# Optimization experiments

Measured on AMD Instinct MI355X. Metric: run time of the kernel, lower is better.

The kernel has to match this reference:

```python
import jax, jax.numpy as jnp
import numpy as np

B, S, D, Q = 8, 4096, 1024, 16  # batch, seq, embed_dim, n_qubits==ffn_dim


def setup_inputs() -> dict:
    key = jax.random.key(0)
    k = jax.random.split(key, 5)
    x = jax.random.normal(k[0], (B, S, D), dtype=jnp.float32)
    W1 = jax.random.normal(k[1], (D, Q), dtype=jnp.float32) * 0.02
    b1 = jnp.zeros((Q,), dtype=jnp.float32)
    theta = jax.random.normal(k[2], (Q,), dtype=jnp.float32)
    W2 = jax.random.normal(k[3], (Q, D), dtype=jnp.float32) * 0.02
    b2 = jnp.zeros((D,), dtype=jnp.float32)
    return {"x": x, "W1": W1, "b1": b1, "theta": theta, "W2": W2, "b2": b2}


def reference(x, W1, b1, theta, W2, b2):
    # linear1 + ReLU (dropout is identity in eval mode)
    h = jax.nn.relu(jnp.einsum("bsd,dq->bsq", x, W1) + b1)  # [B,S,Q] angles
    # QLayer: RY(h_i) then RY(theta_i) on wire i from |0>; rotations on the
    # same wire compose additively and <Z> after RY(a)|0> is cos(a), so
    # MeasureAll(PauliZ) == cos(h + theta) per wire (exact, product state).
    z = jnp.cos(h + theta)  # [B,S,Q]
    # linear2
    return jnp.einsum("bsq,qd->bsd", z, W2) + b2
```

## Files before the change

### kernel.cpp

```cpp
#include <hip/hip_runtime.h>
#include <math.h>
#include <stdint.h>

#define ROWS_TOTAL 32768
#define DDIM 1024
#define QDIM 16

typedef __attribute__((ext_vector_type(8))) short bf16x8;
typedef __attribute__((ext_vector_type(4))) float f32x4;

union ABfrag { uint32_t u[4]; bf16x8 v; };

__device__ __forceinline__ uint32_t packhi(uint32_t a, uint32_t b) {
  return __builtin_amdgcn_perm(b, a, 0x07060302u);
}

#define ZTPB 512
#define ZWPB 8
#define ZNBLOCKS (ROWS_TOTAL / 16)

__global__ __launch_bounds__(ZTPB, 4)
void z_kernel(const float* __restrict__ x, const float* __restrict__ W1,
              const float* __restrict__ b1, const float* __restrict__ theta,
              float* __restrict__ z, int zstride) {
  const int t    = threadIdx.x;
  const int lane = t & 63;
  const int wid  = t >> 6;
  const int g    = lane >> 4;
  const int q5   = lane & 15;

  __shared__ __align__(16) float xs[16][DDIM];
  __shared__ __align__(16) float red[ZWPB][64][4];

  const int row0 = blockIdx.x * 16;
  const int kb   = wid * 128;

  const float bq = b1[q5];
  const float tq = theta[q5];

  float wf[4][8];
#pragma unroll
  for (int s = 0; s < 4; ++s) {
    const float* wp = W1 + (size_t)(kb + 32 * s + 4 * g) * QDIM + q5;
#pragma unroll
    for (int j = 0; j < 4; ++j) wf[s][j] = wp[(size_t)j * QDIM];
#pragma unroll
    for (int j = 0; j < 4; ++j) wf[s][4 + j] = wp[(size_t)(16 + j) * QDIM];
  }

  f32x4 st[8];
  {
    const int rs = 2 * wid;
#pragma unroll
    for (int rr = 0; rr < 2; ++rr) {
      const float* xp = x + (size_t)(row0 + rs + rr) * DDIM;
#pragma unroll
      for (int p = 0; p < 4; ++p)
        st[rr * 4 + p] = __builtin_nontemporal_load(
            reinterpret_cast<const f32x4*>(xp + 4 * (64 * p + lane)));
    }
#pragma unroll
    for (int rr = 0; rr < 2; ++rr) {
      const int r = rs + rr;
#pragma unroll
      for (int p = 0; p < 4; ++p) {
        const int u = 64 * p + lane;
        *reinterpret_cast<f32x4*>(&xs[r][4 * (u ^ (r & 7))]) = st[rr * 4 + p];
      }
    }
  }

  ABfrag bhi[4], blo[4];
#pragma unroll
  for (int s = 0; s < 4; ++s) {
    uint32_t u[8], lo[8];
#pragma unroll
    for (int j = 0; j < 8; ++j) {
      u[j]  = __float_as_uint(wf[s][j]);
      lo[j] = __float_as_uint(wf[s][j] - __uint_as_float(u[j] & 0xFFFF0000u));
    }
    bhi[s].u[0] = packhi(u[0], u[1]);   bhi[s].u[1] = packhi(u[2], u[3]);
    bhi[s].u[2] = packhi(u[4], u[5]);   bhi[s].u[3] = packhi(u[6], u[7]);
    blo[s].u[0] = packhi(lo[0], lo[1]); blo[s].u[1] = packhi(lo[2], lo[3]);
    blo[s].u[2] = packhi(lo[4], lo[5]); blo[s].u[3] = packhi(lo[6], lo[7]);
  }

  __syncthreads();

  const int rr = lane & 15;
  const int ub = 32 * wid;
  float4 a0[4], a1[4];
#pragma unroll
  for (int s = 0; s < 4; ++s) {
    a0[s] = *reinterpret_cast<const float4*>(
        &xs[rr][4 * ((ub + 8 * s + g) ^ (rr & 7))]);
    a1[s] = *reinterpret_cast<const float4*>(
        &xs[rr][4 * ((ub + 8 * s + 4 + g) ^ (rr & 7))]);
  }

  f32x4 acc = {0.f, 0.f, 0.f, 0.f};
#pragma unroll
  for (int s = 0; s < 4; ++s) {
    const float fv[8] = {a0[s].x, a0[s].y, a0[s].z, a0[s].w,
                         a1[s].x, a1[s].y, a1[s].z, a1[s].w};
    uint32_t u[8], lo[8];
#pragma unroll
    for (int j = 0; j < 8; ++j) {
      u[j]  = __float_as_uint(fv[j]);
      lo[j] = __float_as_uint(fv[j] - __uint_as_float(u[j] & 0xFFFF0000u));
    }
    ABfrag ahi, alo;
    ahi.u[0] = packhi(u[0], u[1]);   ahi.u[1] = packhi(u[2], u[3]);
    ahi.u[2] = packhi(u[4], u[5]);   ahi.u[3] = packhi(u[6], u[7]);
    alo.u[0] = packhi(lo[0], lo[1]); alo.u[1] = packhi(lo[2], lo[3]);
    alo.u[2] = packhi(lo[4], lo[5]); alo.u[3] = packhi(lo[6], lo[7]);

    acc = __builtin_amdgcn_mfma_f32_16x16x32_bf16(ahi.v, bhi[s].v, acc, 0, 0, 0);
    acc = __builtin_amdgcn_mfma_f32_16x16x32_bf16(alo.v, bhi[s].v, acc, 0, 0, 0);
    acc = __builtin_amdgcn_mfma_f32_16x16x32_bf16(ahi.v, blo[s].v, acc, 0, 0, 0);
  }

  *reinterpret_cast<f32x4*>(&red[wid][lane][0]) = acc;
  __syncthreads();

  if (wid == 0) {
    f32x4 s0 = *reinterpret_cast<const f32x4*>(&red[0][lane][0]);
#pragma unroll
    for (int w = 1; w < ZWPB; ++w)
      s0 += *reinterpret_cast<const f32x4*>(&red[w][lane][0]);

    const int r0 = g * 4;
#pragma unroll
    for (int i = 0; i < 4; ++i) {
      const float sv = fmaxf(s0[i] + bq, 0.f) + tq;
      z[(size_t)(row0 + r0 + i) * zstride + q5] = __cosf(sv);
    }
  }
}

#define OTPB 256
#define ORPB 16
#define ONBLOCKS (ROWS_TOTAL / ORPB)

__global__ __launch_bounds__(OTPB, 4)
void o_kernel(const float* z, int zstride, const float* __restrict__ W2,
              const float* __restrict__ b2, float* out) {
  const int t   = threadIdx.x;
  const int col = 4 * t;

  float4 w2r[QDIM];
#pragma unroll
  for (int q = 0; q < QDIM; ++q)
    w2r[q] = *reinterpret_cast<const float4*>(W2 + (size_t)q * DDIM + col);
  const float4 bb = *reinterpret_cast<const float4*>(b2 + col);

  const int row0 = blockIdx.x * ORPB;

  const float* zp0 = z + (size_t)row0 * zstride;
  float4 zc0 = *reinterpret_cast<const float4*>(zp0 + 0);
  float4 zc1 = *reinterpret_cast<const float4*>(zp0 + 4);
  float4 zc2 = *reinterpret_cast<const float4*>(zp0 + 8);
  float4 zc3 = *reinterpret_cast<const float4*>(zp0 + 12);

#pragma unroll
  for (int r = 0; r < ORPB; ++r) {
    float4 zn0 = zc0, zn1 = zc1, zn2 = zc2, zn3 = zc3;
    if (r + 1 < ORPB) {
      const float* znp = z + (size_t)(row0 + r + 1) * zstride;
      zn0 = *reinterpret_cast<const float4*>(znp + 0);
      zn1 = *reinterpret_cast<const float4*>(znp + 4);
      zn2 = *reinterpret_cast<const float4*>(znp + 8);
      zn3 = *reinterpret_cast<const float4*>(znp + 12);
    }

    const float zv[16] = {zc0.x, zc0.y, zc0.z, zc0.w,
                          zc1.x, zc1.y, zc1.z, zc1.w,
                          zc2.x, zc2.y, zc2.z, zc2.w,
                          zc3.x, zc3.y, zc3.z, zc3.w};
    float4 acc = bb;
#pragma unroll
    for (int q = 0; q < QDIM; ++q) {
      acc.x = fmaf(zv[q], w2r[q].x, acc.x);
      acc.y = fmaf(zv[q], w2r[q].y, acc.y);
      acc.z = fmaf(zv[q], w2r[q].z, acc.z);
      acc.w = fmaf(zv[q], w2r[q].w, acc.w);
    }
    *reinterpret_cast<float4*>(out + (size_t)(row0 + r) * DDIM + col) = acc;

    zc0 = zn0; zc1 = zn1; zc2 = zn2; zc3 = zn3;
  }
}

extern "C" void kernel_launch(void* const* d_in, const int* in_sizes, int n_in,
                              void* d_out, int out_size, void* d_ws, size_t ws_size,
                              hipStream_t stream) {
  const float* x     = (const float*)d_in[0];
  const float* W1    = (const float*)d_in[1];
  const float* b1    = (const float*)d_in[2];
  const float* theta = (const float*)d_in[3];
  const float* W2    = (const float*)d_in[4];
  const float* b2    = (const float*)d_in[5];
  float* out = (float*)d_out;

  const size_t zbytes = (size_t)ROWS_TOTAL * QDIM * sizeof(float);
  float* zbuf;
  int zstride;
  if (d_ws != nullptr && ws_size >= zbytes) {
    zbuf = (float*)d_ws;
    zstride = QDIM;
  } else {
    zbuf = out;
    zstride = DDIM;
  }

  z_kernel<<<dim3(ZNBLOCKS), dim3(ZTPB), 0, stream>>>(x, W1, b1, theta, zbuf, zstride);
  o_kernel<<<dim3(ONBLOCKS), dim3(OTPB), 0, stream>>>(zbuf, zstride, W2, b2, out);
}
```

Baseline: 56.13 us.

## Process four row tiles per block with register-staged prefetch of next x tile

```diff
diff --git a/kernel.cpp b/kernel.cpp
--- a/kernel.cpp
+++ b/kernel.cpp
@@ -17,7 +17,8 @@
 
 #define ZTPB 512
 #define ZWPB 8
-#define ZNBLOCKS (ROWS_TOTAL / 16)
+#define ZTILES 4
+#define ZNBLOCKS (ROWS_TOTAL / (16 * ZTILES))
 
 __global__ __launch_bounds__(ZTPB, 4)
 void z_kernel(const float* __restrict__ x, const float* __restrict__ W1,
@@ -32,33 +33,51 @@
   __shared__ __align__(16) float xs[16][DDIM];
   __shared__ __align__(16) float red[ZWPB][64][4];
 
-  const int row0 = blockIdx.x * 16;
-  const int kb   = wid * 128;
+  const int tile0 = blockIdx.x * ZTILES;
+  const int kb    = wid * 128;
 
   const float bq = b1[q5];
   const float tq = theta[q5];
 
-  float wf[4][8];
-#pragma unroll
-  for (int s = 0; s < 4; ++s) {
-    const float* wp = W1 + (size_t)(kb + 32 * s + 4 * g) * QDIM + q5;
-#pragma unroll
-    for (int j = 0; j < 4; ++j) wf[s][j] = wp[(size_t)j * QDIM];
-#pragma unroll
-    for (int j = 0; j < 4; ++j) wf[s][4 + j] = wp[(size_t)(16 + j) * QDIM];
-  }
-
+  ABfrag bhi[4], blo[4];
+  {
+    float wf[4][8];
+#pragma unroll
+    for (int s = 0; s < 4; ++s) {
+      const float* wp = W1 + (size_t)(kb + 32 * s + 4 * g) * QDIM + q5;
+#pragma unroll
+      for (int j = 0; j < 4; ++j) wf[s][j] = wp[(size_t)j * QDIM];
+#pragma unroll
+      for (int j = 0; j < 4; ++j) wf[s][4 + j] = wp[(size_t)(16 + j) * QDIM];
+    }
+#pragma unroll
+    for (int s = 0; s < 4; ++s) {
+      uint32_t u[8], lo[8];
+#pragma unroll
+      for (int j = 0; j < 8; ++j) {
+        u[j]  = __float_as_uint(wf[s][j]);
+        lo[j] = __float_as_uint(wf[s][j] - __uint_as_float(u[j] & 0xFFFF0000u));
+      }
+      bhi[s].u[0] = packhi(u[0], u[1]);   bhi[s].u[1] = packhi(u[2], u[3]);
+      bhi[s].u[2] = packhi(u[4], u[5]);   bhi[s].u[3] = packhi(u[6], u[7]);
+      blo[s].u[0] = packhi(lo[0], lo[1]); blo[s].u[1] = packhi(lo[2], lo[3]);
+      blo[s].u[2] = packhi(lo[4], lo[5]); blo[s].u[3] = packhi(lo[6], lo[7]);
+    }
+  }
+
+  const int rs = 2 * wid;
   f32x4 st[8];
-  {
-    const int rs = 2 * wid;
+  auto load_tile = [&](int tile) {
 #pragma unroll
     for (int rr = 0; rr < 2; ++rr) {
-      const float* xp = x + (size_t)(row0 + rs + rr) * DDIM;
+      const float* xp = x + (size_t)(tile * 16 + rs + rr) * DDIM;
 #pragma unroll
       for (int p = 0; p < 4; ++p)
-        st[rr * 4 + p] = __builtin_nontemporal_load(
-            reinterpret_cast<const f32x4*>(xp + 4 * (64 * p + lane)));
-    }
+        st[rr * 4 + p] =
+            *reinterpret_cast<const f32x4*>(xp + 4 * (64 * p + lane));
+    }
+  };
+  auto store_tile = [&]() {
 #pragma unroll
     for (int rr = 0; rr < 2; ++rr) {
       const int r = rs + rr;
@@ -68,72 +87,71 @@
         *reinterpret_cast<f32x4*>(&xs[r][4 * (u ^ (r & 7))]) = st[rr * 4 + p];
       }
     }
-  }
-
-  ABfrag bhi[4], blo[4];
-#pragma unroll
-  for (int s = 0; s < 4; ++s) {
-    uint32_t u[8], lo[8];
-#pragma unroll
-    for (int j = 0; j < 8; ++j) {
-      u[j]  = __float_as_uint(wf[s][j]);
-      lo[j] = __float_as_uint(wf[s][j] - __uint_as_float(u[j] & 0xFFFF0000u));
-    }
-    bhi[s].u[0] = packhi(u[0], u[1]);   bhi[s].u[1] = packhi(u[2], u[3]);
-    bhi[s].u[2] = packhi(u[4], u[5]);   bhi[s].u[3] = packhi(u[6], u[7]);
-    blo[s].u[0] = packhi(lo[0], lo[1]); blo[s].u[1] = packhi(lo[2], lo[3]);
-    blo[s].u[2] = packhi(lo[4], lo[5]); blo[s].u[3] = packhi(lo[6], lo[7]);
-  }
-
-  __syncthreads();
-
-  const int rr = lane & 15;
+  };
+
+  load_tile(tile0);
+  store_tile();
+  load_tile(tile0 + 1);
+  asm volatile("s_waitcnt lgkmcnt(0)" ::: "memory");
+  __builtin_amdgcn_s_barrier();
+
   const int ub = 32 * wid;
-  float4 a0[4], a1[4];
-#pragma unroll
-  for (int s = 0; s < 4; ++s) {
-    a0[s] = *reinterpret_cast<const float4*>(
-        &xs[rr][4 * ((ub + 8 * s + g) ^ (rr & 7))]);
-    a1[s] = *reinterpret_cast<const float4*>(
-        &xs[rr][4 * ((ub + 8 * s + 4 + g) ^ (rr & 7))]);
-  }
-
-  f32x4 acc = {0.f, 0.f, 0.f, 0.f};
-#pragma unroll
-  for (int s = 0; s < 4; ++s) {
-    const float fv[8] = {a0[s].x, a0[s].y, a0[s].z, a0[s].w,
-                         a1[s].x, a1[s].y, a1[s].z, a1[s].w};
-    uint32_t u[8], lo[8];
-#pragma unroll
-    for (int j = 0; j < 8; ++j) {
-      u[j]  = __float_as_uint(fv[j]);
-      lo[j] = __float_as_uint(fv[j] - __uint_as_float(u[j] & 0xFFFF0000u));
-    }
-    ABfrag ahi, alo;
-    ahi.u[0] = packhi(u[0], u[1]);   ahi.u[1] = packhi(u[2], u[3]);
-    ahi.u[2] = packhi(u[4], u[5]);   ahi.u[3] = packhi(u[6], u[7]);
-    alo.u[0] = packhi(lo[0], lo[1]); alo.u[1] = packhi(lo[2], lo[3]);
-    alo.u[2] = packhi(lo[4], lo[5]); alo.u[3] = packhi(lo[6], lo[7]);
-
-    acc = __builtin_amdgcn_mfma_f32_16x16x32_bf16(ahi.v, bhi[s].v, acc, 0, 0, 0);
-    acc = __builtin_amdgcn_mfma_f32_16x16x32_bf16(alo.v, bhi[s].v, acc, 0, 0, 0);
-    acc = __builtin_amdgcn_mfma_f32_16x16x32_bf16(ahi.v, blo[s].v, acc, 0, 0, 0);
-  }
-
-  *reinterpret_cast<f32x4*>(&red[wid][lane][0]) = acc;
-  __syncthreads();
-
-  if (wid == 0) {
-    f32x4 s0 = *reinterpret_cast<const f32x4*>(&red[0][lane][0]);
-#pragma unroll
-    for (int w = 1; w < ZWPB; ++w)
-      s0 += *reinterpret_cast<const f32x4*>(&red[w][lane][0]);
-
-    const int r0 = g * 4;
-#pragma unroll
-    for (int i = 0; i < 4; ++i) {
-      const float sv = fmaxf(s0[i] + bq, 0.f) + tq;
-      z[(size_t)(row0 + r0 + i) * zstride + q5] = __cosf(sv);
+  const int rr_f = lane & 15;
+  const int swz = rr_f & 7;
+
+  for (int tt = 0; tt < ZTILES; ++tt) {
+    const int row0 = (tile0 + tt) * 16;
+
+    float4 a0[4], a1[4];
+#pragma unroll
+    for (int s = 0; s < 4; ++s) {
+      a0[s] = *reinterpret_cast<const float4*>(
+          &xs[rr_f][4 * ((ub + 8 * s + g) ^ swz)]);
+      a1[s] = *reinterpret_cast<const float4*>(
+          &xs[rr_f][4 * ((ub + 8 * s + 4 + g) ^ swz)]);
+    }
+    asm volatile("s_waitcnt lgkmcnt(0)" ::: "memory");
+    __builtin_amdgcn_s_barrier();
+
+    if (tt + 1 < ZTILES) {
+      store_tile();
+      if (tt + 2 < ZTILES) load_tile(tile0 + tt + 2);
+    }
+
+    f32x4 acc = {0.f, 0.f, 0.f, 0.f};
+#pragma unroll
+    for (int s = 0; s < 4; ++s) {
+      const float fv[8] = {a0[s].x, a0[s].y, a0[s].z, a0[s].w,
+                           a1[s].x, a1[s].y, a1[s].z, a1[s].w};
+      uint32_t u[8], lo[8];
+#pragma unroll
+      for (int j = 0; j < 8; ++j) {
+        u[j]  = __float_as_uint(fv[j]);
+        lo[j] = __float_as_uint(fv[j] - __uint_as_float(u[j] & 0xFFFF0000u));
+      }
+      ABfrag ahi, alo;
+      ahi.u[0] = packhi(u[0], u[1]);   ahi.u[1] = packhi(u[2], u[3]);
+      ahi.u[2] = packhi(u[4], u[5]);   ahi.u[3] = packhi(u[6], u[7]);
+      alo.u[0] = packhi(lo[0], lo[1]); alo.u[1] = packhi(lo[2], lo[3]);
+      alo.u[2] = packhi(lo[4], lo[5]); alo.u[3] = packhi(lo[6], lo[7]);
+
+      acc = __builtin_amdgcn_mfma_f32_16x16x32_bf16(ahi.v, bhi[s].v, acc, 0, 0, 0);
+      acc = __builtin_amdgcn_mfma_f32_16x16x32_bf16(alo.v, bhi[s].v, acc, 0, 0, 0);
+      acc = __builtin_amdgcn_mfma_f32_16x16x32_bf16(ahi.v, blo[s].v, acc, 0, 0, 0);
+    }
+
+    *reinterpret_cast<f32x4*>(&red[wid][lane][0]) = acc;
+    asm volatile("s_waitcnt lgkmcnt(0)" ::: "memory");
+    __builtin_amdgcn_s_barrier();
+
+    if (lane < 32) {
+      const int rr = rs + ((lane >> 4) & 1);
+      const int l2 = (rr >> 2) * 16 + q5;
+      float ssum = 0.f;
+#pragma unroll
+      for (int j = 0; j < ZWPB; ++j) ssum += red[j][l2][rr & 3];
+      const float sv = fmaxf(ssum + bq, 0.f) + tq;
+      z[(size_t)(row0 + rr) * zstride + q5] = __cosf(sv);
     }
   }
 }
```

Result: slower. 63.91 us (+13.9%).
